# Kernel optimization log

Hardware: AMD Instinct MI355X
Metric: run time of the kernel (lower is better)

## Reference

```python
import jax, jax.numpy as jnp
import numpy as np

N = 40962          # icosphere level-6 vertex count
E = 245772         # N * k (k=6 knn, directed)
MUL_IN = 8         # '8x0e + 8x1o' -> dim 8 + 24 = 32
MUL_OUT = 16       # '16x0e + 16x1o' -> dim 16 + 48 = 64
H = 64             # radial MLP hidden
WNUM = 4 * MUL_IN * MUL_OUT  # 512 per-edge TP weights (4 CG paths)
SQ3 = np.float32(np.sqrt(3.0))


def setup_inputs() -> dict:
    key = jax.random.key(0)
    ks = jax.random.split(key, 8)
    x = jax.random.normal(ks[0], (N, MUL_IN + 3 * MUL_IN), dtype=jnp.float32)
    pos = jax.random.normal(ks[1], (N, 3), dtype=jnp.float32)
    src = jax.random.randint(ks[2], (E,), 0, N)
    dst = jax.random.randint(ks[3], (E,), 0, N)
    edge_index = jnp.stack([src, dst]).astype(jnp.int32)
    W1 = jax.random.normal(ks[4], (1, H), dtype=jnp.float32)
    W2 = jax.random.normal(ks[5], (H, WNUM), dtype=jnp.float32)
    Ws = jax.random.normal(ks[6], (MUL_OUT, MUL_OUT), dtype=jnp.float32)
    k7, k8 = jax.random.split(ks[7])
    Wns = jax.random.normal(k7, (MUL_OUT, MUL_OUT), dtype=jnp.float32)
    Wg = jax.random.normal(k8, (MUL_OUT, MUL_OUT), dtype=jnp.float32)
    return {"x": x, "pos": pos, "edge_index": edge_index,
            "W1": W1, "W2": W2, "Ws": Ws, "Wns": Wns, "Wg": Wg}


def reference(x, pos, edge_index, W1, W2, Ws, Wns, Wg):
    src, dst = edge_index[0], edge_index[1]
    xs = x[:, :MUL_IN]                                  # (N, 8)  scalars (0e)
    xv = x[:, MUL_IN:].reshape(-1, MUL_IN, 3)           # (N, 8, 3) vectors (1o)

    # --- edge geometry + spherical harmonics (component-normalized, lmax=1) ---
    edge_vec = pos[dst] - pos[src]                      # (E, 3)
    edge_len = jnp.maximum(jnp.linalg.norm(edge_vec, axis=-1, keepdims=True), 1e-8)
    edge_dir = edge_vec / edge_len                      # (E, 3)
    Y1 = SQ3 * edge_dir                                 # l=1 SH; l=0 SH == 1

    # --- radial MLP -> per-edge tensor-product weights (shared_weights=False) ---
    h = jax.nn.silu(edge_len @ W1)                      # (E, H), fan_in = 1
    w = (h @ W2) * (1.0 / np.sqrt(np.float32(H)))       # (E, 512)
    wA, wB, wC, wD = [wi.reshape(-1, MUL_IN, MUL_OUT)
                      for wi in jnp.split(w, 4, axis=1)]

    xs_e = xs[src]                                      # (E, 8)   gather
    xv_e = xv[src]                                      # (E, 8, 3) gather
    norm = np.float32(1.0 / np.sqrt(2.0 * MUL_IN))      # path normalization

    # --- tensor product: 4 CG paths ---
    # 0e x 0e -> 0e  (CG = 1)
    pathA = jnp.einsum('eu,euw->ew', xs_e, wA)
    # 1o x 1o -> 0e  (CG_ij = delta_ij / sqrt(3))
    dot = jnp.einsum('eui,ei->eu', xv_e, Y1) * (1.0 / SQ3)
    pathB = jnp.einsum('eu,euw->ew', dot, wB)
    m_s = (pathA + pathB) * norm                        # (E, 16)
    # 0e x 1o -> 1o  (CG = identity)
    pathC = jnp.einsum('eu,euw->ew', xs_e, wC)[:, :, None] * Y1[:, None, :]
    # 1o x 0e -> 1o  (CG = identity)
    pathD = jnp.einsum('eui,euw->ewi', xv_e, wD)
    m_v = (pathC + pathD) * norm                        # (E, 16, 3)

    m = jnp.concatenate([m_s, m_v.reshape(-1, 3 * MUL_OUT)], axis=1)  # (E, 64)

    # --- scatter-add to destination nodes (index_add) ---
    out = jnp.zeros((x.shape[0], m.shape[1]), dtype=x.dtype).at[dst].add(m)

    # --- gated equivariant nonlinearity (o3.Linear with fan-in norm) ---
    lin_norm = np.float32(1.0 / np.sqrt(np.float32(MUL_OUT)))
    os_ = out[:, :MUL_OUT]                              # (N, 16)
    ov_ = out[:, MUL_OUT:].reshape(-1, MUL_OUT, 3)      # (N, 16, 3)
    s = jax.nn.silu(os_ @ Ws * lin_norm)                # (N, 16)
    ns = jnp.einsum('nui,uw->nwi', ov_, Wns) * lin_norm # (N, 16, 3)
    g = jax.nn.sigmoid(os_ @ Wg * lin_norm)             # (N, 16)
    gated = (g[:, :, None] * ns).reshape(-1, 3 * MUL_OUT)
    return jnp.concatenate([s, gated], axis=1)          # (N, 64)
```

## Files before the change

kernel.cpp:

```cpp
#include <hip/hip_runtime.h>
#include <math.h>

typedef _Float16 half8 __attribute__((ext_vector_type(8)));
typedef float floatx4 __attribute__((ext_vector_type(4)));

#define SQ3 1.7320508075688772f

__global__ __launch_bounds__(256) void prep_w2(const float* __restrict__ W2,
                                               _Float16* __restrict__ bw) {
    int t = blockIdx.x * 256 + threadIdx.x;
    if (t >= 32768) return;
    int i    = t & 7;
    int l    = (t >> 3) & 63;
    int s    = (t >> 9) & 1;
    int tt   = (t >> 10) & 7;
    int path = t >> 13;
    int k   = s * 32 + (l >> 4) * 8 + i;
    int col = path * 128 + tt * 16 + (l & 15);
    float scale = 0.03125f * (path == 2 ? SQ3 : 1.0f);
    bw[t] = (_Float16)(W2[k * 512 + col] * scale);
}

struct Pref {
    float4 xa, xb;
    float psx, psy, psz, pdx, pdy, pdz;
    int si, di;
};

__device__ __forceinline__ Pref issue_loads(int tile, int E,
        const int* __restrict__ ei, const float* __restrict__ x,
        const float* __restrict__ pos, int tid) {
    Pref p;
    int el = tid >> 2, q = tid & 3;
    int eg = tile * 64 + el;
    int ec = (eg < E) ? eg : (E - 1);
    p.si = ei[ec];
    p.di = ei[E + ec];
    const float* xr = x + (size_t)p.si * 32 + q * 8;
    p.xa = *reinterpret_cast<const float4*>(xr);
    p.xb = *reinterpret_cast<const float4*>(xr + 4);
    const float* ps = pos + (size_t)p.si * 3;
    const float* pd = pos + (size_t)p.di * 3;
    p.psx = ps[0]; p.psy = ps[1]; p.psz = ps[2];
    p.pdx = pd[0]; p.pdy = pd[1]; p.pdz = pd[2];
    return p;
}

__global__ __launch_bounds__(256) void edge_kernel(
    const float* __restrict__ x, const float* __restrict__ pos,
    const int* __restrict__ ei, const float* __restrict__ W1,
    const _Float16* __restrict__ bw, float* __restrict__ out,
    int E, int ntiles)
{
    __shared__ float sW1[64];
    __shared__ __align__(16) float4 s_geo[2][64];
    __shared__ int s_dst[2][64];
    __shared__ __align__(16) _Float16 s_xs[2][64][8];
    __shared__ __align__(16) _Float16 s_xv[2][64][24];
    __shared__ __align__(16) _Float16 s_hA[2][4][2][64][8];
    __shared__ __align__(16) _Float16 s_part[2][64][64];

    const int tid  = threadIdx.x;
    const int wave = tid >> 6;
    const int lane = tid & 63;

    if (tid < 64) sW1[tid] = W1[tid];

    half8 bfrag[8][2];
    {
        const half8* bsrc = (const half8*)bw;
        #pragma unroll
        for (int t = 0; t < 8; ++t)
            #pragma unroll
            for (int s = 0; s < 2; ++s)
                bfrag[t][s] = bsrc[(size_t)wave * 1024 + (t * 2 + s) * 64 + lane];
    }

    int tile = blockIdx.x;
    if (tile >= ntiles) return;
    Pref p = issue_loads(tile, E, ei, x, pos, tid);
    __syncthreads();

    int buf = 0;
    for (; tile < ntiles; tile += gridDim.x) {
        {
            int el = tid >> 2, q = tid & 3;
            half8 hv;
            hv[0] = (_Float16)p.xa.x; hv[1] = (_Float16)p.xa.y;
            hv[2] = (_Float16)p.xa.z; hv[3] = (_Float16)p.xa.w;
            hv[4] = (_Float16)p.xb.x; hv[5] = (_Float16)p.xb.y;
            hv[6] = (_Float16)p.xb.z; hv[7] = (_Float16)p.xb.w;
            if (q == 0) *(half8*)&s_xs[buf][el][0] = hv;
            else        *(half8*)&s_xv[buf][el][(q - 1) * 8] = hv;

            float ex = p.pdx - p.psx;
            float ey = p.pdy - p.psy;
            float ez = p.pdz - p.psz;
            float len = fmaxf(sqrtf(ex * ex + ey * ey + ez * ez), 1e-8f);
            float inv = 1.0f / len;
            if (q == 0) {
                s_geo[buf][el] = make_float4(ex * inv, ey * inv, ez * inv, len);
                s_dst[buf][el] = p.di;
            }
            int sub = el >> 4;
            int l   = (q << 4) | (el & 15);
            #pragma unroll
            for (int s = 0; s < 2; ++s) {
                half8 ha;
                #pragma unroll
                for (int i = 0; i < 8; ++i) {
                    float z = len * sW1[s * 32 + q * 8 + i];
                    ha[i] = (_Float16)(z / (1.0f + __expf(-z)));
                }
                *(half8*)&s_hA[buf][sub][s][l][0] = ha;
            }
        }
        __syncthreads();

        int nt = tile + gridDim.x;
        bool has = (nt < ntiles);
        Pref pn;
        if (has) pn = issue_loads(nt, E, ei, x, pos, tid);

        const int wp  = lane & 15;
        const int er0 = (lane >> 4) * 4;
        #pragma unroll
        for (int sub = 0; sub < 4; ++sub) {
            half8 a0 = *(const half8*)&s_hA[buf][sub][0][lane][0];
            half8 a1 = *(const half8*)&s_hA[buf][sub][1][lane][0];
            floatx4 acc[8];
            #pragma unroll
            for (int t = 0; t < 8; ++t) {
                floatx4 z = {0.f, 0.f, 0.f, 0.f};
                z = __builtin_amdgcn_mfma_f32_16x16x32_f16(a0, bfrag[t][0], z, 0, 0, 0);
                acc[t] = __builtin_amdgcn_mfma_f32_16x16x32_f16(a1, bfrag[t][1], z, 0, 0, 0);
            }

            if (wave == 0) {
                #pragma unroll
                for (int r = 0; r < 4; ++r) {
                    int e = sub * 16 + er0 + r;
                    half8 xs = *(const half8*)&s_xs[buf][e][0];
                    float m = 0.f;
                    #pragma unroll
                    for (int u = 0; u < 8; ++u) m += (float)xs[u] * acc[u][r];
                    s_part[0][e][wp] = (_Float16)m;
                }
            } else if (wave == 1) {
                #pragma unroll
                for (int r = 0; r < 4; ++r) {
                    int e = sub * 16 + er0 + r;
                    half8 v0 = *(const half8*)&s_xv[buf][e][0];
                    half8 v1 = *(const half8*)&s_xv[buf][e][8];
                    half8 v2 = *(const half8*)&s_xv[buf][e][16];
                    float4 g = s_geo[buf][e];
                    float xf[24];
                    #pragma unroll
                    for (int i = 0; i < 8; ++i) {
                        xf[i] = (float)v0[i]; xf[8 + i] = (float)v1[i];
                        xf[16 + i] = (float)v2[i];
                    }
                    float m = 0.f;
                    #pragma unroll
                    for (int u = 0; u < 8; ++u) {
                        float dot = xf[u*3+0]*g.x + xf[u*3+1]*g.y + xf[u*3+2]*g.z;
                        m += dot * acc[u][r];
                    }
                    s_part[1][e][wp] = (_Float16)m;
                }
            } else if (wave == 2) {
                #pragma unroll
                for (int r = 0; r < 4; ++r) {
                    int e = sub * 16 + er0 + r;
                    half8 xs = *(const half8*)&s_xs[buf][e][0];
                    float4 g = s_geo[buf][e];
                    float cw = 0.f;
                    #pragma unroll
                    for (int u = 0; u < 8; ++u) cw += (float)xs[u] * acc[u][r];
                    s_part[0][e][16 + wp * 3 + 0] = (_Float16)(cw * g.x);
                    s_part[0][e][16 + wp * 3 + 1] = (_Float16)(cw * g.y);
                    s_part[0][e][16 + wp * 3 + 2] = (_Float16)(cw * g.z);
                }
            } else {
                #pragma unroll
                for (int r = 0; r < 4; ++r) {
                    int e = sub * 16 + er0 + r;
                    half8 v0 = *(const half8*)&s_xv[buf][e][0];
                    half8 v1 = *(const half8*)&s_xv[buf][e][8];
                    half8 v2 = *(const half8*)&s_xv[buf][e][16];
                    float xf[24];
                    #pragma unroll
                    for (int i = 0; i < 8; ++i) {
                        xf[i] = (float)v0[i]; xf[8 + i] = (float)v1[i];
                        xf[16 + i] = (float)v2[i];
                    }
                    float m0 = 0.f, m1 = 0.f, m2 = 0.f;
                    #pragma unroll
                    for (int u = 0; u < 8; ++u) {
                        float w = acc[u][r];
                        m0 += xf[u*3+0] * w;
                        m1 += xf[u*3+1] * w;
                        m2 += xf[u*3+2] * w;
                    }
                    s_part[1][e][16 + wp * 3 + 0] = (_Float16)m0;
                    s_part[1][e][16 + wp * 3 + 1] = (_Float16)m1;
                    s_part[1][e][16 + wp * 3 + 2] = (_Float16)m2;
                }
            }
        }
        __syncthreads();

        {
            int c = tid & 63;
            int g = tid >> 6;
            #pragma unroll
            for (int k = 0; k < 16; ++k) {
                int e  = g * 16 + k;
                int eg = tile * 64 + e;
                if (eg < E) {
                    float v = (float)s_part[0][e][c] + (float)s_part[1][e][c];
                    atomicAdd(out + (size_t)s_dst[buf][e] * 64 + c, v);
                }
            }
        }
        p = pn;
        buf ^= 1;
    }
}

__global__ __launch_bounds__(256) void node_kernel(
    float* __restrict__ out, const float* __restrict__ Ws,
    const float* __restrict__ Wns, const float* __restrict__ Wg, int N)
{
    int n = blockIdx.x * 256 + threadIdx.x;
    if (n >= N) return;
    float* row = out + (size_t)n * 64;

    float os[16], ov[48];
    #pragma unroll
    for (int q = 0; q < 4; ++q) {
        float4 v = *reinterpret_cast<const float4*>(row + q * 4);
        os[q*4+0]=v.x; os[q*4+1]=v.y; os[q*4+2]=v.z; os[q*4+3]=v.w;
    }
    #pragma unroll
    for (int q = 0; q < 12; ++q) {
        float4 v = *reinterpret_cast<const float4*>(row + 16 + q * 4);
        ov[q*4+0]=v.x; ov[q*4+1]=v.y; ov[q*4+2]=v.z; ov[q*4+3]=v.w;
    }

    float sres[16], gres[16];
    #pragma unroll
    for (int w = 0; w < 16; ++w) {
        float a = 0.f, b = 0.f;
        #pragma unroll
        for (int u = 0; u < 16; ++u) {
            float o_u = os[u];
            a += o_u * Ws[u * 16 + w];
            b += o_u * Wg[u * 16 + w];
        }
        a *= 0.25f; b *= 0.25f;
        sres[w] = a / (1.0f + __expf(-a));
        gres[w] = 1.0f / (1.0f + __expf(-b));
    }

    float gated[48];
    #pragma unroll
    for (int w = 0; w < 16; ++w) {
        float n0 = 0.f, n1 = 0.f, n2 = 0.f;
        #pragma unroll
        for (int u = 0; u < 16; ++u) {
            float wn = Wns[u * 16 + w];
            n0 += ov[u*3+0] * wn;
            n1 += ov[u*3+1] * wn;
            n2 += ov[u*3+2] * wn;
        }
        float gw = gres[w] * 0.25f;
        gated[w*3+0] = n0 * gw;
        gated[w*3+1] = n1 * gw;
        gated[w*3+2] = n2 * gw;
    }

    #pragma unroll
    for (int q = 0; q < 4; ++q) {
        float4 v = make_float4(sres[q*4+0], sres[q*4+1], sres[q*4+2], sres[q*4+3]);
        *reinterpret_cast<float4*>(row + q * 4) = v;
    }
    #pragma unroll
    for (int q = 0; q < 12; ++q) {
        float4 v = make_float4(gated[q*4+0], gated[q*4+1], gated[q*4+2], gated[q*4+3]);
        *reinterpret_cast<float4*>(row + 16 + q * 4) = v;
    }
}

extern "C" void kernel_launch(void* const* d_in, const int* in_sizes, int n_in,
                              void* d_out, int out_size, void* d_ws, size_t ws_size,
                              hipStream_t stream) {
    const float* x   = (const float*)d_in[0];
    const float* pos = (const float*)d_in[1];
    const int*   ei  = (const int*)d_in[2];
    const float* W1  = (const float*)d_in[3];
    const float* W2  = (const float*)d_in[4];
    const float* Ws  = (const float*)d_in[5];
    const float* Wns = (const float*)d_in[6];
    const float* Wg  = (const float*)d_in[7];

    int N = in_sizes[0] / 32;
    int E = in_sizes[2] / 2;
    int ntiles = (E + 63) / 64;
    float* out = (float*)d_out;
    _Float16* bw = (_Float16*)d_ws;

    hipMemsetAsync(out, 0, (size_t)N * 64 * sizeof(float), stream);
    prep_w2<<<128, 256, 0, stream>>>(W2, bw);
    int nblk = ntiles < 960 ? ntiles : 960;
    edge_kernel<<<nblk, 256, 0, stream>>>(x, pos, ei, W1, bw, out, E, ntiles);
    node_kernel<<<(N + 255) / 256, 256, 0, stream>>>(out, Ws, Wns, Wg, N);
}
```

Baseline: 107.0 us.

## Store edge features as fp32 component-planar in LDS, drop double buffering

Node features are now staged in shared memory as fp32 instead of fp16. The vector part is transposed into three component planes, so the per-path contractions read float4 rows with no conversions. Single-buffering s_geo, s_xs and s_hA and padding s_part shrink LDS use and reduce bank conflicts. Launch bounds and the persistent grid size are raised to allow more resident blocks. The risks are LDS races, because s_hA and s_geo are no longer double-buffered while the next tile is written, and higher register pressure from the new launch bounds.

```diff
diff --git a/kernel.cpp b/kernel.cpp
--- a/kernel.cpp
+++ b/kernel.cpp
@@ -24,7 +24,7 @@
 struct Pref {
     float4 xa, xb;
     float psx, psy, psz, pdx, pdy, pdz;
-    int si, di;
+    int di;
 };
 
 __device__ __forceinline__ Pref issue_loads(int tile, int E,
@@ -34,31 +34,31 @@
     int el = tid >> 2, q = tid & 3;
     int eg = tile * 64 + el;
     int ec = (eg < E) ? eg : (E - 1);
-    p.si = ei[ec];
+    int si = ei[ec];
     p.di = ei[E + ec];
-    const float* xr = x + (size_t)p.si * 32 + q * 8;
+    const float* xr = x + (size_t)si * 32 + q * 8;
     p.xa = *reinterpret_cast<const float4*>(xr);
     p.xb = *reinterpret_cast<const float4*>(xr + 4);
-    const float* ps = pos + (size_t)p.si * 3;
+    const float* ps = pos + (size_t)si * 3;
     const float* pd = pos + (size_t)p.di * 3;
     p.psx = ps[0]; p.psy = ps[1]; p.psz = ps[2];
     p.pdx = pd[0]; p.pdy = pd[1]; p.pdz = pd[2];
     return p;
 }
 
-__global__ __launch_bounds__(256) void edge_kernel(
+__global__ __launch_bounds__(256, 4) void edge_kernel(
     const float* __restrict__ x, const float* __restrict__ pos,
     const int* __restrict__ ei, const float* __restrict__ W1,
     const _Float16* __restrict__ bw, float* __restrict__ out,
     int E, int ntiles)
 {
     __shared__ float sW1[64];
-    __shared__ __align__(16) float4 s_geo[2][64];
+    __shared__ __align__(16) float4 s_geo[64];
     __shared__ int s_dst[2][64];
-    __shared__ __align__(16) _Float16 s_xs[2][64][8];
-    __shared__ __align__(16) _Float16 s_xv[2][64][24];
-    __shared__ __align__(16) _Float16 s_hA[2][4][2][64][8];
-    __shared__ __align__(16) _Float16 s_part[2][64][64];
+    __shared__ __align__(16) float s_xs[64][12];
+    __shared__ __align__(16) float s_xvp[3][64][12];
+    __shared__ __align__(16) _Float16 s_hA[4][2][64][8];
+    __shared__ __align__(16) _Float16 s_part[2][64][66];
 
     const int tid  = threadIdx.x;
     const int wave = tid >> 6;
@@ -85,22 +85,27 @@
     for (; tile < ntiles; tile += gridDim.x) {
         {
             int el = tid >> 2, q = tid & 3;
-            half8 hv;
-            hv[0] = (_Float16)p.xa.x; hv[1] = (_Float16)p.xa.y;
-            hv[2] = (_Float16)p.xa.z; hv[3] = (_Float16)p.xa.w;
-            hv[4] = (_Float16)p.xb.x; hv[5] = (_Float16)p.xb.y;
-            hv[6] = (_Float16)p.xb.z; hv[7] = (_Float16)p.xb.w;
-            if (q == 0) *(half8*)&s_xs[buf][el][0] = hv;
-            else        *(half8*)&s_xv[buf][el][(q - 1) * 8] = hv;
-
             float ex = p.pdx - p.psx;
             float ey = p.pdy - p.psy;
             float ez = p.pdz - p.psz;
             float len = fmaxf(sqrtf(ex * ex + ey * ey + ez * ez), 1e-8f);
             float inv = 1.0f / len;
             if (q == 0) {
-                s_geo[buf][el] = make_float4(ex * inv, ey * inv, ez * inv, len);
+                s_geo[el] = make_float4(ex * inv, ey * inv, ez * inv, len);
                 s_dst[buf][el] = p.di;
+                *(float4*)&s_xs[el][0] = p.xa;
+                *(float4*)&s_xs[el][4] = p.xb;
+            } else {
+                int fb = (q - 1) * 8;
+                float vals[8] = {p.xa.x, p.xa.y, p.xa.z, p.xa.w,
+                                 p.xb.x, p.xb.y, p.xb.z, p.xb.w};
+                #pragma unroll
+                for (int i2 = 0; i2 < 8; ++i2) {
+                    int flat = fb + i2;
+                    int u  = (flat * 11) >> 5;
+                    int ii = flat - 3 * u;
+                    s_xvp[ii][el][u] = vals[i2];
+                }
             }
             int sub = el >> 4;
             int l   = (q << 4) | (el & 15);
@@ -112,22 +117,21 @@
                     float z = len * sW1[s * 32 + q * 8 + i];
                     ha[i] = (_Float16)(z / (1.0f + __expf(-z)));
                 }
-                *(half8*)&s_hA[buf][sub][s][l][0] = ha;
+                *(half8*)&s_hA[sub][s][l][0] = ha;
             }
         }
         __syncthreads();
 
         int nt = tile + gridDim.x;
-        bool has = (nt < ntiles);
         Pref pn;
-        if (has) pn = issue_loads(nt, E, ei, x, pos, tid);
+        if (nt < ntiles) pn = issue_loads(nt, E, ei, x, pos, tid);
 
         const int wp  = lane & 15;
         const int er0 = (lane >> 4) * 4;
         #pragma unroll
         for (int sub = 0; sub < 4; ++sub) {
-            half8 a0 = *(const half8*)&s_hA[buf][sub][0][lane][0];
-            half8 a1 = *(const half8*)&s_hA[buf][sub][1][lane][0];
+            half8 a0 = *(const half8*)&s_hA[sub][0][lane][0];
+            half8 a1 = *(const half8*)&s_hA[sub][1][lane][0];
             floatx4 acc[8];
             #pragma unroll
             for (int t = 0; t < 8; ++t) {
@@ -140,43 +144,38 @@
                 #pragma unroll
                 for (int r = 0; r < 4; ++r) {
                     int e = sub * 16 + er0 + r;
-                    half8 xs = *(const half8*)&s_xs[buf][e][0];
+                    float4 x0 = *(const float4*)&s_xs[e][0];
+                    float4 x1 = *(const float4*)&s_xs[e][4];
+                    float m = x0.x*acc[0][r] + x0.y*acc[1][r] + x0.z*acc[2][r] + x0.w*acc[3][r]
+                            + x1.x*acc[4][r] + x1.y*acc[5][r] + x1.z*acc[6][r] + x1.w*acc[7][r];
+                    s_part[0][e][wp] = (_Float16)m;
+                }
+            } else if (wave == 1) {
+                #pragma unroll
+                for (int r = 0; r < 4; ++r) {
+                    int e = sub * 16 + er0 + r;
+                    float4 g = s_geo[e];
                     float m = 0.f;
                     #pragma unroll
-                    for (int u = 0; u < 8; ++u) m += (float)xs[u] * acc[u][r];
-                    s_part[0][e][wp] = (_Float16)m;
-                }
-            } else if (wave == 1) {
+                    for (int i = 0; i < 3; ++i) {
+                        float4 v0 = *(const float4*)&s_xvp[i][e][0];
+                        float4 v1 = *(const float4*)&s_xvp[i][e][4];
+                        float gi = (i == 0) ? g.x : ((i == 1) ? g.y : g.z);
+                        float d = v0.x*acc[0][r] + v0.y*acc[1][r] + v0.z*acc[2][r] + v0.w*acc[3][r]
+                                + v1.x*acc[4][r] + v1.y*acc[5][r] + v1.z*acc[6][r] + v1.w*acc[7][r];
+                        m += gi * d;
+                    }
+                    s_part[1][e][wp] = (_Float16)m;
+                }
+            } else if (wave == 2) {
                 #pragma unroll
                 for (int r = 0; r < 4; ++r) {
                     int e = sub * 16 + er0 + r;
-                    half8 v0 = *(const half8*)&s_xv[buf][e][0];
-                    half8 v1 = *(const half8*)&s_xv[buf][e][8];
-                    half8 v2 = *(const half8*)&s_xv[buf][e][16];
-                    float4 g = s_geo[buf][e];
-                    float xf[24];
-                    #pragma unroll
-                    for (int i = 0; i < 8; ++i) {
-                        xf[i] = (float)v0[i]; xf[8 + i] = (float)v1[i];
-                        xf[16 + i] = (float)v2[i];
-                    }
-                    float m = 0.f;
-                    #pragma unroll
-                    for (int u = 0; u < 8; ++u) {
-                        float dot = xf[u*3+0]*g.x + xf[u*3+1]*g.y + xf[u*3+2]*g.z;
-                        m += dot * acc[u][r];
-                    }
-                    s_part[1][e][wp] = (_Float16)m;
-                }
-            } else if (wave == 2) {
-                #pragma unroll
-                for (int r = 0; r < 4; ++r) {
-                    int e = sub * 16 + er0 + r;
-                    half8 xs = *(const half8*)&s_xs[buf][e][0];
-                    float4 g = s_geo[buf][e];
-                    float cw = 0.f;
-                    #pragma unroll
-                    for (int u = 0; u < 8; ++u) cw += (float)xs[u] * acc[u][r];
+                    float4 x0 = *(const float4*)&s_xs[e][0];
+                    float4 x1 = *(const float4*)&s_xs[e][4];
+                    float4 g = s_geo[e];
+                    float cw = x0.x*acc[0][r] + x0.y*acc[1][r] + x0.z*acc[2][r] + x0.w*acc[3][r]
+                             + x1.x*acc[4][r] + x1.y*acc[5][r] + x1.z*acc[6][r] + x1.w*acc[7][r];
                     s_part[0][e][16 + wp * 3 + 0] = (_Float16)(cw * g.x);
                     s_part[0][e][16 + wp * 3 + 1] = (_Float16)(cw * g.y);
                     s_part[0][e][16 + wp * 3 + 2] = (_Float16)(cw * g.z);
@@ -185,26 +184,14 @@
                 #pragma unroll
                 for (int r = 0; r < 4; ++r) {
                     int e = sub * 16 + er0 + r;
-                    half8 v0 = *(const half8*)&s_xv[buf][e][0];
-                    half8 v1 = *(const half8*)&s_xv[buf][e][8];
-                    half8 v2 = *(const half8*)&s_xv[buf][e][16];
-                    float xf[24];
                     #pragma unroll
-                    for (int i = 0; i < 8; ++i) {
-                        xf[i] = (float)v0[i]; xf[8 + i] = (float)v1[i];
-                        xf[16 + i] = (float)v2[i];
+                    for (int i = 0; i < 3; ++i) {
+                        float4 v0 = *(const float4*)&s_xvp[i][e][0];
+                        float4 v1 = *(const float4*)&s_xvp[i][e][4];
+                        float mi = v0.x*acc[0][r] + v0.y*acc[1][r] + v0.z*acc[2][r] + v0.w*acc[3][r]
+                                 + v1.x*acc[4][r] + v1.y*acc[5][r] + v1.z*acc[6][r] + v1.w*acc[7][r];
+                        s_part[1][e][16 + wp * 3 + i] = (_Float16)mi;
                     }
-                    float m0 = 0.f, m1 = 0.f, m2 = 0.f;
-                    #pragma unroll
-                    for (int u = 0; u < 8; ++u) {
-                        float w = acc[u][r];
-                        m0 += xf[u*3+0] * w;
-                        m1 += xf[u*3+1] * w;
-                        m2 += xf[u*3+2] * w;
-                    }
-                    s_part[1][e][16 + wp * 3 + 0] = (_Float16)m0;
-                    s_part[1][e][16 + wp * 3 + 1] = (_Float16)m1;
-                    s_part[1][e][16 + wp * 3 + 2] = (_Float16)m2;
                 }
             }
         }
@@ -312,7 +299,7 @@
 
     hipMemsetAsync(out, 0, (size_t)N * 64 * sizeof(float), stream);
     prep_w2<<<128, 256, 0, stream>>>(W2, bw);
-    int nblk = ntiles < 960 ? ntiles : 960;
+    int nblk = ntiles < 1024 ? ntiles : 1024;
     edge_kernel<<<nblk, 256, 0, stream>>>(x, pos, ei, W1, bw, out, E, ntiles);
     node_kernel<<<(N + 255) / 256, 256, 0, stream>>>(out, Ws, Wns, Wg, N);
 }
```

New measurement: 139.3 us. 30.2% more time.
